# Kernel tuning notes

Measured on AMD Instinct MI355X. Metric: run time of the kernel, lower is better.

Reference implementation:

```python
import jax, jax.numpy as jnp
import numpy as np

DIM = 2048
H = 16           # n_heads
KV = 4           # n_kv_heads
G = H // KV      # gqa factor
CQ = 128         # q_compressed_dim
QN, QR = 96, 32  # q nope / rope head dims
CKV = 128        # kv_compressed_dim
KN, KR = 64, 64  # k nope / rope head dims
VD = 256         # v_head_dim
THETA = 10000.0


def _t5_layer_norm(x, gamma, eps=1e-5):
    mu = jnp.mean(x, axis=-1, keepdims=True)
    var = jnp.var(x, axis=-1, keepdims=True)
    return (x - mu) * jax.lax.rsqrt(var + eps) * gamma


def _rope(x):
    # x: [B, H, S, D] with interleaved even/odd rotation, positions = arange(S)
    S, D = x.shape[-2], x.shape[-1]
    inv_freq = 1.0 / THETA ** (jnp.arange(0, D, 2, dtype=jnp.float32) / D)
    ang = jnp.arange(S, dtype=jnp.float32)[:, None] * inv_freq  # [S, D/2]
    cos = jnp.cos(ang).astype(x.dtype)
    sin = jnp.sin(ang).astype(x.dtype)
    xe, xo = x[..., ::2], x[..., 1::2]
    re = xe * cos - xo * sin
    ro = xe * sin + xo * cos
    return jnp.stack((re, ro), axis=-1).reshape(x.shape)


def setup_inputs() -> dict:
    key = jax.random.key(0)
    ks = jax.random.split(key, 7)
    s = 0.02
    return {
        "x": jax.random.normal(ks[0], (2, 2048, DIM), dtype=jnp.float32),
        "w_dq": jax.random.normal(ks[1], (DIM, CQ), dtype=jnp.float32) * s,
        "gamma_q": jnp.ones((CQ,), dtype=jnp.float32),
        "w_uq": jax.random.normal(ks[2], (CQ, H * (QN + QR)), dtype=jnp.float32) * s,
        "w_dkv": jax.random.normal(ks[3], (DIM, CKV + KR), dtype=jnp.float32) * s,
        "gamma_kv": jnp.ones((CKV,), dtype=jnp.float32),
        "w_ukv": jax.random.normal(ks[4], (CKV, KV * (KN + VD)), dtype=jnp.float32) * s,
        "w_o": jax.random.normal(ks[5], (H * VD, DIM), dtype=jnp.float32) * s,
    }


def reference(x, w_dq, gamma_q, w_uq, w_dkv, gamma_kv, w_ukv, w_o):
    B, S, _ = x.shape
    # low-rank Q path
    cq = _t5_layer_norm(x @ w_dq, gamma_q)                     # [B,S,CQ]
    q = cq @ w_uq                                              # [B,S,H*(QN+QR)]
    q_nope = q[..., : H * QN].reshape(B, S, H, QN).transpose(0, 2, 1, 3)
    q_rope = q[..., H * QN :].reshape(B, S, H, QR).transpose(0, 2, 1, 3)
    q_rope = _rope(q_rope)
    q_states = jnp.concatenate((q_nope, q_rope), axis=-1)      # [B,H,S,QN+QR]

    # low-rank KV path + decoupled shared rope key
    ckv_kr = x @ w_dkv                                         # [B,S,CKV+KR]
    ckv = _t5_layer_norm(ckv_kr[..., :CKV], gamma_kv)
    k_rope = _rope(ckv_kr[..., CKV:][:, None, :, :])           # [B,1,S,KR]
    kv = ckv @ w_ukv                                           # [B,S,KV*(KN+VD)]
    k_nope = kv[..., : KV * KN].reshape(B, S, KV, KN).transpose(0, 2, 1, 3)
    v_states = kv[..., KV * KN :].reshape(B, S, KV, VD).transpose(0, 2, 1, 3)
    k_states = jnp.concatenate(
        (k_nope, jnp.broadcast_to(k_rope, (B, KV, S, KR))), axis=-1
    )                                                          # [B,KV,S,KN+KR]

    # grouped-query attention: broadcast kv heads instead of materializing repeats
    dqk = QN + QR  # == KN + KR == 128
    qg = q_states.reshape(B, KV, G, S, dqk)
    scores = jnp.einsum("bgrqd,bgkd->bgrqk", qg, k_states) / jnp.sqrt(
        jnp.asarray(dqk, dtype=x.dtype)
    )
    causal = jnp.triu(jnp.ones((S, S), dtype=bool), k=1)
    scores = jnp.where(causal, -jnp.inf, scores)
    attn = jax.nn.softmax(scores, axis=-1)
    out = jnp.einsum("bgrqk,bgkv->bgrqv", attn, v_states)      # [B,KV,G,S,VD]
    out = out.reshape(B, H, S, VD).transpose(0, 2, 1, 3).reshape(B, S, H * VD)
    return out @ w_o
```

## Files before the change

kernel.cpp:

```cpp
#include <hip/hip_runtime.h>
#include <hip/hip_bf16.h>
#include <math.h>

#define DIM   2048
#define S_LEN 2048
#define BATCH 2
#define NH    16
#define NKV   4
#define CQ_   128
#define QN_   96
#define QR_   32
#define CKV_  128
#define KN_   64
#define KR_   64
#define VD_   256
#define ROWS_TOT (BATCH*S_LEN)
#define QK_SCALE 0.08838834764831845f
#define LOG2E    1.4426950408889634f

typedef __attribute__((ext_vector_type(8)))  short short8;
typedef __attribute__((ext_vector_type(4)))  short short4v;
typedef __attribute__((ext_vector_type(4)))  float float4v;
typedef __attribute__((ext_vector_type(16))) float float16v;
typedef __attribute__((ext_vector_type(4)))  int   int4v;

__device__ inline short f2bf(float x) {
    union { __hip_bfloat16 h; short s; } u;
    u.h = __float2bfloat16(x);
    return u.s;
}

__device__ __forceinline__ void gl_lds16(const short* g, short* lds) {
    __builtin_amdgcn_global_load_lds(
        (const __attribute__((address_space(1))) unsigned int*)(g),
        (__attribute__((address_space(3))) unsigned int*)(lds),
        16, 0, 0);
}


__global__ __launch_bounds__(256)
void kprep_all(const float* __restrict__ w_o, const float* __restrict__ w_uq,
               const float* __restrict__ w_ukv, const float* __restrict__ w_dq,
               const float* __restrict__ w_dkv,
               short* __restrict__ w_oT, short* __restrict__ w_uqT,
               short* __restrict__ w_ukvT, short* __restrict__ wdT,
               float* __restrict__ tq, float* __restrict__ tk)
{
    const int bid = blockIdx.x, tid = threadIdx.x;
    if (bid >= 2312) {
        int gid = (bid - 2312) * 256 + tid;
        int spos = gid / 48, e = gid - spos * 48;
        if (e < 16) {
            float inv = powf(10000.f, -(float)(2 * e) / 32.f);
            float sn, c; sincosf((float)spos * inv, &sn, &c);
            tq[(spos * 16 + e) * 2 + 0] = c;
            tq[(spos * 16 + e) * 2 + 1] = sn;
        } else {
            int i2 = e - 16;
            float inv = powf(10000.f, -(float)(2 * i2) / 64.f);
            float sn, c; sincosf((float)spos * inv, &sn, &c);
            tk[(spos * 32 + i2) * 2 + 0] = c;
            tk[(spos * 32 + i2) * 2 + 1] = sn;
        }
        return;
    }

    __shared__ float tf[64][65];
    int lb, nct, R; short* dst;
    if (bid < 2048)      { lb = bid;        nct = 32; R = 4096; dst = w_oT;   }
    else if (bid < 2112) { lb = bid - 2048; nct = 32; R = 128;  dst = w_uqT;  }
    else if (bid < 2152) { lb = bid - 2112; nct = 20; R = 128;  dst = w_ukvT; }
    else                 { lb = bid - 2152; nct = 5;  R = 2048; dst = wdT;    }
    const int ct = lb % nct, rt = lb / nct;
    const int r0 = rt * 64, c0 = ct * 64;
    const float* src; int stride, nbase;
    if (bid < 2048)      { src = w_o;   stride = 2048; nbase = c0; }
    else if (bid < 2112) { src = w_uq;  stride = 2048; nbase = c0; }
    else if (bid < 2152) { src = w_ukv; stride = 1280; nbase = c0; }
    else if (ct < 2)     { src = w_dq;  stride = 128;  nbase = c0; }
    else                 { src = w_dkv; stride = 192;  nbase = c0 - 128; }

    #pragma unroll
    for (int u4 = 0; u4 < 4; ++u4) {
        int u = u4 * 256 + tid;
        int kr = u >> 4, nc = (u & 15) * 4;
        float4 v = *reinterpret_cast<const float4*>(&src[(size_t)(r0 + kr) * stride + nbase + nc]);
        tf[kr][nc + 0] = v.x; tf[kr][nc + 1] = v.y;
        tf[kr][nc + 2] = v.z; tf[kr][nc + 3] = v.w;
    }
    __syncthreads();
    #pragma unroll
    for (int u2 = 0; u2 < 2; ++u2) {
        int u = u2 * 256 + tid;
        int nr = u >> 3, kc8 = (u & 7) * 8;
        short8 o;
        #pragma unroll
        for (int j = 0; j < 8; ++j) o[j] = f2bf(tf[kc8 + j][nr]);
        *reinterpret_cast<short8*>(&dst[(size_t)(c0 + nr) * R + r0 + kc8]) = o;
    }
}

__global__ __launch_bounds__(256)
void k1_mfma(const float* __restrict__ x, const short* __restrict__ wdT,
             const float* __restrict__ gamma_q, const float* __restrict__ gamma_kv,
             const float* __restrict__ tk,
             short* __restrict__ cq_bf, short* __restrict__ ckv_bf,
             float* __restrict__ kr_rope)
{
    __shared__ float ys[16][321];
    __shared__ float st[16][4];
    const int tid = threadIdx.x, lane = tid & 63, w = tid >> 6;
    const int g = lane >> 4, l15 = lane & 15;
    const int m0 = blockIdx.x * 16;
    const int wn0 = w * 80;

    float4v acc[5];
    #pragma unroll
    for (int nj = 0; nj < 5; ++nj) acc[nj] = (float4v){0.f, 0.f, 0.f, 0.f};

    const float* arow = x + (size_t)(m0 + l15) * 2048 + g * 8;
    for (int ks = 0; ks < 64; ++ks) {
        float4 a0 = *reinterpret_cast<const float4*>(arow + ks * 32);
        float4 a1 = *reinterpret_cast<const float4*>(arow + ks * 32 + 4);
        short8 a;
        a[0] = f2bf(a0.x); a[1] = f2bf(a0.y); a[2] = f2bf(a0.z); a[3] = f2bf(a0.w);
        a[4] = f2bf(a1.x); a[5] = f2bf(a1.y); a[6] = f2bf(a1.z); a[7] = f2bf(a1.w);
        #pragma unroll
        for (int nj = 0; nj < 5; ++nj) {
            short8 bf = *reinterpret_cast<const short8*>(
                wdT + (size_t)(wn0 + nj * 16 + l15) * 2048 + ks * 32 + g * 8);
            acc[nj] = __builtin_amdgcn_mfma_f32_16x16x32_bf16(a, bf, acc[nj], 0, 0, 0);
        }
    }

    #pragma unroll
    for (int nj = 0; nj < 5; ++nj)
        #pragma unroll
        for (int r = 0; r < 4; ++r)
            ys[g * 4 + r][wn0 + nj * 16 + l15] = acc[nj][r];
    __syncthreads();

    if (tid < 32) {
        int row = tid >> 1, seg = tid & 1, base = seg * 128;
        float s1 = 0.f, s2 = 0.f;
        for (int j = 0; j < 128; ++j) { float v = ys[row][base + j]; s1 += v; s2 += v * v; }
        float mu  = s1 * (1.f / 128.f);
        float var = s2 * (1.f / 128.f) - mu * mu;
        st[row][seg * 2 + 0] = mu;
        st[row][seg * 2 + 1] = rsqrtf(var + 1e-5f);
    }
    __syncthreads();

    for (int i = tid; i < 16 * 320; i += 256) {
        int row = i / 320, col = i - row * 320;
        int r = m0 + row, spos = r & (S_LEN - 1);
        float v = ys[row][col];
        if (col < 128) {
            cq_bf[(size_t)r * CQ_ + col] =
                f2bf((v - st[row][0]) * st[row][1] * gamma_q[col] * (QK_SCALE * LOG2E));
        } else if (col < 256) {
            ckv_bf[(size_t)r * CKV_ + (col - 128)] =
                f2bf((v - st[row][2]) * st[row][3] * gamma_kv[col - 128]);
        } else {
            int d = col - 256, i2 = d >> 1;
            float xe = ys[row][256 + (d & ~1)];
            float xo = ys[row][256 + (d | 1)];
            float c  = tk[(spos * 32 + i2) * 2 + 0];
            float sn = tk[(spos * 32 + i2) * 2 + 1];
            kr_rope[(size_t)r * KR_ + d] = (d & 1) ? (xe * sn + xo * c)
                                                   : (xe * c - xo * sn);
        }
    }
}

__global__ __launch_bounds__(256)
void k2_mfma(const short* __restrict__ cq_bf, const short* __restrict__ w_uqT,
             const float* __restrict__ tq, short* __restrict__ q_states)
{
    const int tid = threadIdx.x, lane = tid & 63, w = tid >> 6;
    const int g = lane >> 4, l15 = lane & 15;
    const int bm = blockIdx.x >> 1, ns = blockIdx.x & 1;
    const int m0 = bm * 16;
    const int nb = ns * 1024 + w * 256;

    short8 af[4];
    #pragma unroll
    for (int ks = 0; ks < 4; ++ks)
        af[ks] = *reinterpret_cast<const short8*>(
            cq_bf + (size_t)(m0 + l15) * 128 + ks * 32 + g * 8);

    float4v acc[16];
    #pragma unroll
    for (int nj = 0; nj < 16; ++nj) acc[nj] = (float4v){0.f, 0.f, 0.f, 0.f};

    #pragma unroll
    for (int ks = 0; ks < 4; ++ks)
        #pragma unroll
        for (int nj = 0; nj < 16; ++nj) {
            short8 bf = *reinterpret_cast<const short8*>(
                w_uqT + (size_t)(nb + nj * 16 + l15) * 128 + ks * 32 + g * 8);
            acc[nj] = __builtin_amdgcn_mfma_f32_16x16x32_bf16(af[ks], bf, acc[nj], 0, 0, 0);
        }

    #pragma unroll
    for (int nj = 0; nj < 16; ++nj) {
        int j = nb + nj * 16 + l15;
        if (j < NH * QN_) {
            int h = j / QN_, d = j - h * QN_;
            #pragma unroll
            for (int r = 0; r < 4; ++r) {
                int rg = m0 + g * 4 + r, bb = rg >> 11, spos = rg & (S_LEN - 1);
                q_states[(((size_t)bb * NH + h) * S_LEN + spos) * 128 + d] =
                    f2bf(acc[nj][r]);
            }
        } else {
            int jj = j - NH * QN_;
            int h = jj >> 5, d = jj & 31, i2 = d >> 1;
            #pragma unroll
            for (int r = 0; r < 4; ++r) {
                int rg = m0 + g * 4 + r, bb = rg >> 11, spos = rg & (S_LEN - 1);
                float v = acc[nj][r];
                float p = __shfl_xor(v, 1, 64);
                float c  = tq[(spos * 16 + i2) * 2 + 0];
                float sn = tq[(spos * 16 + i2) * 2 + 1];
                float out = (d & 1) ? (p * sn + v * c) : (v * c - p * sn);
                q_states[(((size_t)bb * NH + h) * S_LEN + spos) * 128 + QN_ + d] =
                    f2bf(out);
            }
        }
    }
}

__global__ __launch_bounds__(256)
void k3_mfma(const short* __restrict__ ckv_bf, const short* __restrict__ w_ukvT,
             const float* __restrict__ kr_rope,
             short* __restrict__ k_frag, short* __restrict__ v_states)
{
    const int tid = threadIdx.x, lane = tid & 63, w = tid >> 6;
    const int g = lane >> 4, l15 = lane & 15;
    const int m0 = blockIdx.x * 16;
    const int nb = w * 320;

    short8 af[4];
    #pragma unroll
    for (int ks = 0; ks < 4; ++ks)
        af[ks] = *reinterpret_cast<const short8*>(
            ckv_bf + (size_t)(m0 + l15) * 128 + ks * 32 + g * 8);

    float4v acc[20];
    #pragma unroll
    for (int nj = 0; nj < 20; ++nj) acc[nj] = (float4v){0.f, 0.f, 0.f, 0.f};

    #pragma unroll
    for (int ks = 0; ks < 4; ++ks)
        #pragma unroll
        for (int nj = 0; nj < 20; ++nj) {
            short8 bf = *reinterpret_cast<const short8*>(
                w_ukvT + (size_t)(nb + nj * 16 + l15) * 128 + ks * 32 + g * 8);
            acc[nj] = __builtin_amdgcn_mfma_f32_16x16x32_bf16(af[ks], bf, acc[nj], 0, 0, 0);
        }

    #pragma unroll
    for (int nj = 0; nj < 20; ++nj) {
        int j = nb + nj * 16 + l15;
        if (j < NKV * KN_) {
            int kvh = j >> 6, d = j & 63;
            int stf = d >> 4, hif = (d >> 3) & 1, jo = d & 7;
            #pragma unroll
            for (int r = 0; r < 4; ++r) {
                int rg = m0 + g * 4 + r, bb = rg >> 11, spos = rg & (S_LEN - 1);
                int bk = bb * NKV + kvh;
                size_t idx = ((size_t)(bk * 32 + (spos >> 6)) * 1024
                              + ((spos >> 5) & 1) * 512 + stf * 64 + hif * 32
                              + (spos & 31)) * 8 + jo;
                k_frag[idx] = f2bf(acc[nj][r]);
            }
        } else {
            int jj = j - NKV * KN_;
            int kvh = jj >> 8, d = jj & 255;
            #pragma unroll
            for (int r = 0; r < 4; ++r) {
                int rg = m0 + g * 4 + r, bb = rg >> 11, spos = rg & (S_LEN - 1);
                v_states[(((size_t)bb * NKV + kvh) * S_LEN + spos) * VD_ + d] =
                    f2bf(acc[nj][r]);
            }
        }
    }

    for (int i = tid; i < 16 * KR_; i += 256) {
        int rr = i >> 6, dd = i & 63;
        int rg = m0 + rr, bb = rg >> 11, spos = rg & (S_LEN - 1);
        short vv = f2bf(kr_rope[(size_t)rg * KR_ + dd]);
        int d = 64 + dd;
        int stf = d >> 4, hif = (d >> 3) & 1, jo = d & 7;
        size_t ubase = ((size_t)(spos >> 6)) * 1024
                       + ((spos >> 5) & 1) * 512 + stf * 64 + hif * 32 + (spos & 31);
        #pragma unroll
        for (int kvh = 0; kvh < NKV; ++kvh) {
            int bk = bb * NKV + kvh;
            k_frag[((size_t)bk * 32 * 1024 + ubase) * 8 + jo] = vv;
        }
    }
}

__global__ __launch_bounds__(256)
void k3t_transpose_v(const short* __restrict__ v, short* __restrict__ v_frag)
{
    __shared__ short t[64][66];
    const int tid = threadIdx.x;
    const int vtile = blockIdx.x & 3;
    const int stile = (blockIdx.x >> 2) & 31;
    const int bk    = blockIdx.x >> 7;

    const short* src = v + ((size_t)bk * S_LEN + stile * 64) * VD_ + vtile * 64;
    #pragma unroll
    for (int u2 = 0; u2 < 2; ++u2) {
        int u = u2 * 256 + tid;
        int srow = u >> 3, vc8 = (u & 7) * 8;
        short8 val = *reinterpret_cast<const short8*>(src + (size_t)srow * VD_ + vc8);
        #pragma unroll
        for (int j = 0; j < 8; ++j) t[srow][vc8 + j] = val[j];
    }
    __syncthreads();
    short* dstbase = v_frag + (size_t)(bk * 32 + stile) * 16384;
    #pragma unroll
    for (int u2 = 0; u2 < 2; ++u2) {
        int u = u2 * 256 + tid;
        int vr = u >> 3, sc8 = (u & 7) * 8;
        short8 o;
        #pragma unroll
        for (int j = 0; j < 8; ++j) o[j] = t[sc8 + j][vr];
        int d = vtile * 64 + vr;
        int dt = d >> 5, l31d = d & 31;
        int half = sc8 >> 5, ksf = (sc8 >> 4) & 1, hif = (sc8 >> 3) & 1;
        size_t idx16 = (size_t)dt * 256 + half * 128 + ksf * 64 + hif * 32 + l31d;
        *reinterpret_cast<short8*>(dstbase + idx16 * 8) = o;
    }
}

__global__ __launch_bounds__(512, 1)
void k4_attn_mfma(const short* __restrict__ q_states,
                  const short* __restrict__ k_frag,
                  const short* __restrict__ v_frag,
                  short* __restrict__ attn_out)
{
    __shared__ __align__(16) short ks_lds[3][8192];
    __shared__ __align__(16) short vt_lds[2][16384];

    const int tid = threadIdx.x, lane = tid & 63, w = tid >> 6;
    const int l31 = lane & 31, hi = lane >> 5;
    const int g = w & 3, h = w >> 2;
    const int bid = blockIdx.x;
    const int qt = (bid < 256) ? (15 - (bid >> 5)) : (7 - ((bid - 256) >> 5));
    const int bh = bid & 31;
    const int h_head = bh & 15, b = bh >> 4, kvh = h_head >> 2;
    const int bk = b * NKV + kvh;

    const short* kfbase = k_frag + (size_t)bk * 32 * 8192;
    const short* vfbase = v_frag + (size_t)bk * 32 * 16384;

    const int qrow0 = qt * 128 + g * 32;
    const int qglob = qrow0 + l31;

    short8 qcur[8];
    {
        const short* qr = q_states +
            (((size_t)b * NH + h_head) * S_LEN + qrow0 + l31) * 128 + hi * 8;
        #pragma unroll
        for (int st = 0; st < 8; ++st)
            qcur[st] = *reinterpret_cast<const short8*>(qr + st * 16);
    }

    float16v o[8];
    #pragma unroll
    for (int dt = 0; dt < 8; ++dt)
        #pragma unroll
        for (int r = 0; r < 16; ++r) o[dt][r] = 0.f;
    float mreg = -1e30f, lreg = 0.f;

    const int nkt = 2 * (qt + 1);

    auto issueK = [&](int kt, int bufi) {
        const short* src = kfbase + (size_t)kt * 8192;
        #pragma unroll
        for (int i = 0; i < 2; ++i) {
            int c = w * 2 + i;
            gl_lds16(src + c * 512 + lane * 8, &ks_lds[bufi][c * 512]);
        }
    };
    auto issueV = [&](int kt, int bufi) {
        const short* src = vfbase + (size_t)kt * 16384;
        #pragma unroll
        for (int i = 0; i < 4; ++i) {
            int c = w * 4 + i;
            gl_lds16(src + c * 512 + lane * 8, &vt_lds[bufi][c * 512]);
        }
    };

    issueK(0, 0);
    issueV(0, 0);
    issueK(1, 1);

    for (int seq = 0; seq < nkt; ++seq) {
        if (seq < nkt - 1) { asm volatile("s_waitcnt vmcnt(2)" ::: "memory"); }
        else               { asm volatile("s_waitcnt vmcnt(0)" ::: "memory"); }
        __builtin_amdgcn_s_barrier();
        __builtin_amdgcn_sched_barrier(0);

        if (seq + 1 < nkt) issueV(seq + 1, (seq + 1) & 1);
        if (seq + 2 < nkt) issueK(seq + 2, (seq + 2) % 3);

        const int kvb = seq * 64 + h * 32;
        if (kvb <= qrow0 + 31) {
            const short* kbuf = &ks_lds[seq % 3][h * 4096];
            float16v s;
            #pragma unroll
            for (int r = 0; r < 16; ++r) s[r] = 0.f;
            __builtin_amdgcn_s_setprio(1);
            #pragma unroll
            for (int st = 0; st < 8; ++st) {
                short8 kf = *reinterpret_cast<const short8*>(kbuf + st * 512 + lane * 8);
                s = __builtin_amdgcn_mfma_f32_32x32x16_bf16(kf, qcur[st], s, 0, 0, 0);
            }
            __builtin_amdgcn_s_setprio(0);

            if (kvb + 31 > qglob - (l31 == 31 ? 0 : 0)) {
                #pragma unroll
                for (int r = 0; r < 16; ++r) {
                    int kc = kvb + ((r & 3) + 8 * (r >> 2) + 4 * hi);
                    if (kc > qglob) s[r] = -1e30f;
                }
            }

            float mx = s[0];
            #pragma unroll
            for (int r = 1; r < 16; ++r) mx = fmaxf(mx, s[r]);
            mx = fmaxf(mx, __shfl_xor(mx, 32, 64));
            bool need = mx > mreg + 8.f;
            if (__ballot(need)) {
                float mnew = fmaxf(mreg, mx);
                float corr = exp2f(mreg - mnew);
                mreg = mnew;
                lreg *= corr;
                #pragma unroll
                for (int dt = 0; dt < 8; ++dt)
                    #pragma unroll
                    for (int r = 0; r < 16; ++r) o[dt][r] *= corr;
            }
            #pragma unroll
            for (int r = 0; r < 16; ++r) s[r] = exp2f(s[r] - mreg);
            float ps = 0.f;
            #pragma unroll
            for (int r = 0; r < 16; ++r) ps += s[r];
            ps += __shfl_xor(ps, 32, 64);
            lreg += ps;

            const short* vbuf = &vt_lds[seq & 1][h * 1024];
            __builtin_amdgcn_s_setprio(1);
            #pragma unroll
            for (int ks = 0; ks < 2; ++ks) {
                const int rb = ks * 8;
                int c01, c23, c45, c67;
                asm("v_cvt_pk_bf16_f32 %0, %1, %2" : "=v"(c01) : "v"(s[rb+0]), "v"(s[rb+1]));
                asm("v_cvt_pk_bf16_f32 %0, %1, %2" : "=v"(c23) : "v"(s[rb+2]), "v"(s[rb+3]));
                asm("v_cvt_pk_bf16_f32 %0, %1, %2" : "=v"(c45) : "v"(s[rb+4]), "v"(s[rb+5]));
                asm("v_cvt_pk_bf16_f32 %0, %1, %2" : "=v"(c67) : "v"(s[rb+6]), "v"(s[rb+7]));
                asm("v_permlane32_swap_b32 %0, %1" : "+v"(c01), "+v"(c45));
                asm("v_permlane32_swap_b32 %0, %1" : "+v"(c23), "+v"(c67));
                union { int4v i4; short8 s8; } u_;
                u_.i4.x = c01; u_.i4.y = c23; u_.i4.z = c45; u_.i4.w = c67;
                short8 pa = u_.s8;
                #pragma unroll
                for (int dt = 0; dt < 8; ++dt) {
                    short8 vf = *reinterpret_cast<const short8*>(
                        vbuf + dt * 2048 + ks * 512 + lane * 8);
                    o[dt] = __builtin_amdgcn_mfma_f32_32x32x16_bf16(vf, pa, o[dt], 0, 0, 0);
                }
            }
            __builtin_amdgcn_s_setprio(0);
        }
    }

    __syncthreads();
    {
        float* mlb = (float*)(&ks_lds[0][0]);
        mlb[w * 64 + lane] = mreg;
        mlb[512 + w * 64 + lane] = lreg;
    }
    __syncthreads();
    float s0f = 0.f, s1f = 0.f;
    if (h == 0) {
        float* mlb = (float*)(&ks_lds[0][0]);
        float m1 = mlb[(w + 4) * 64 + lane];
        float l1 = mlb[512 + (w + 4) * 64 + lane];
        float ms = fmaxf(mreg, m1);
        float c0 = exp2f(mreg - ms), c1 = exp2f(m1 - ms);
        float ls = lreg * c0 + l1 * c1;
        s0f = c0 / ls; s1f = c1 / ls;
    }
    float* cb = (float*)(&ks_lds[0][0]) + 1024;
    short* obase = attn_out + (((size_t)b * S_LEN + qglob) * NH + h_head) * VD_;
    for (int dt = 0; dt < 8; ++dt) {
        __syncthreads();
        if (h == 1) {
            #pragma unroll
            for (int r = 0; r < 16; ++r)
                cb[r * 256 + g * 64 + lane] = o[dt][r];
        }
        __syncthreads();
        if (h == 0) {
            #pragma unroll
            for (int r = 0; r < 16; ++r)
                o[dt][r] = o[dt][r] * s0f + cb[r * 256 + g * 64 + lane] * s1f;
            #pragma unroll
            for (int k4i = 0; k4i < 4; ++k4i) {
                int d0 = dt * 32 + k4i * 8 + hi * 4;
                short4v pk;
                #pragma unroll
                for (int j = 0; j < 4; ++j) pk[j] = f2bf(o[dt][k4i * 4 + j]);
                *reinterpret_cast<short4v*>(obase + d0) = pk;
            }
        }
    }
}

__global__ __launch_bounds__(256)
void k5_gemm_mfma(const short* __restrict__ A,
                  const short* __restrict__ Bt,
                  float* __restrict__ C)
{
    __shared__ __align__(16) short at[128 * 64];
    __shared__ __align__(16) short bt[128 * 64];
    const int tid  = threadIdx.x;
    const int lane = tid & 63;
    const int wid  = tid >> 6;
    const int wm = wid >> 1, wn = wid & 1;
    const int g = lane >> 4, l15 = lane & 15;
    const int wg = (blockIdx.x & 7) * 64 + (blockIdx.x >> 3);
    const int bn = wg & 15, bm = wg >> 4;
    const int m0 = bm * 128, n0 = bn * 128;

    float4v acc[4][4];
    #pragma unroll
    for (int mi = 0; mi < 4; ++mi)
        #pragma unroll
        for (int nj = 0; nj < 4; ++nj) acc[mi][nj] = (float4v){0.f, 0.f, 0.f, 0.f};

    for (int k0 = 0; k0 < 4096; k0 += 64) {
        __syncthreads();
        #pragma unroll
        for (int i = 0; i < 4; ++i) {
            int row = wid * 32 + i * 8 + (lane >> 3);
            int ch  = lane & 7;
            gl_lds16(A + (size_t)(m0 + row) * 4096 + k0 + ((ch ^ (row & 7)) * 8),
                     at + wid * 2048 + i * 512);
            gl_lds16(Bt + (size_t)(n0 + row) * 4096 + k0 + ((ch ^ (row & 7)) * 8),
                     bt + wid * 2048 + i * 512);
        }
        __syncthreads();

        #pragma unroll
        for (int kb = 0; kb < 2; ++kb) {
            short8 af[4], bfr[4];
            #pragma unroll
            for (int mi = 0; mi < 4; ++mi) {
                int row = wm * 64 + mi * 16 + l15;
                af[mi] = *reinterpret_cast<const short8*>(
                    at + row * 64 + (((g + 4 * kb) ^ (row & 7)) * 8));
            }
            #pragma unroll
            for (int nj = 0; nj < 4; ++nj) {
                int row = wn * 64 + nj * 16 + l15;
                bfr[nj] = *reinterpret_cast<const short8*>(
                    bt + row * 64 + (((g + 4 * kb) ^ (row & 7)) * 8));
            }
            #pragma unroll
            for (int mi = 0; mi < 4; ++mi)
                #pragma unroll
                for (int nj = 0; nj < 4; ++nj)
                    acc[mi][nj] = __builtin_amdgcn_mfma_f32_16x16x32_bf16(
                        af[mi], bfr[nj], acc[mi][nj], 0, 0, 0);
        }
    }

    #pragma unroll
    for (int mi = 0; mi < 4; ++mi)
        #pragma unroll
        for (int nj = 0; nj < 4; ++nj)
            #pragma unroll
            for (int r = 0; r < 4; ++r)
                C[(size_t)(m0 + wm * 64 + mi * 16 + g * 4 + r) * DIM + n0 + wn * 64 + nj * 16 + l15] =
                    acc[mi][nj][r];
}

extern "C" void kernel_launch(void* const* d_in, const int* in_sizes, int n_in,
                              void* d_out, int out_size, void* d_ws, size_t ws_size,
                              hipStream_t stream)
{
    const float* x        = (const float*)d_in[0];
    const float* w_dq     = (const float*)d_in[1];
    const float* gamma_q  = (const float*)d_in[2];
    const float* w_uq     = (const float*)d_in[3];
    const float* w_dkv    = (const float*)d_in[4];
    const float* gamma_kv = (const float*)d_in[5];
    const float* w_ukv    = (const float*)d_in[6];
    const float* w_o      = (const float*)d_in[7];
    float* out = (float*)d_out;

    char* ws = (char*)d_ws;
    float* kr_rope  = (float*)(ws);
    short* cq_bf    = (short*)(ws + (1ull  << 20));
    short* ckv_bf   = (short*)(ws + (2ull  << 20));
    float* tq       = (float*)(ws + (3ull  << 20));
    float* tk       = (float*)(ws + (4ull  << 20));
    short* w_uqT    = (short*)(ws + (5ull  << 20));
    short* w_ukvT   = (short*)(ws + (6ull  << 20));
    short* wdT      = (short*)(ws + (7ull  << 20));
    short* q_states = (short*)(ws + (9ull  << 20));
    short* k_frag   = (short*)(ws + (25ull << 20));
    short* v_states = (short*)(ws + (29ull << 20));
    short* v_frag   = (short*)(ws + (37ull << 20));
    short* attn_out = (short*)(ws + (45ull << 20));
    short* w_oT     = (short*)(ws + (77ull << 20));

    kprep_all<<<dim3(2696), dim3(256), 0, stream>>>(
        w_o, w_uq, w_ukv, w_dq, w_dkv, w_oT, w_uqT, w_ukvT, wdT, tq, tk);

    k1_mfma<<<dim3(ROWS_TOT / 16), dim3(256), 0, stream>>>(
        x, wdT, gamma_q, gamma_kv, tk, cq_bf, ckv_bf, kr_rope);

    k2_mfma<<<dim3((ROWS_TOT / 16) * 2), dim3(256), 0, stream>>>(
        cq_bf, w_uqT, tq, q_states);

    k3_mfma<<<dim3(ROWS_TOT / 16), dim3(256), 0, stream>>>(
        ckv_bf, w_ukvT, kr_rope, k_frag, v_states);

    k3t_transpose_v<<<dim3(BATCH * NKV * 32 * 4), dim3(256), 0, stream>>>(
        v_states, v_frag);

    k4_attn_mfma<<<dim3(512), dim3(512), 0, stream>>>(
        q_states, k_frag, v_frag, attn_out);

    k5_gemm_mfma<<<dim3((ROWS_TOT / 128) * (DIM / 128)), dim3(256), 0, stream>>>(
        attn_out, w_oT, out);
}
```

Baseline: 262.5 us.

## Fuse Q/KV up-projections, write V fragments directly, pre-convert x, split QK MFMA chains

Several changes land together. x is converted to bf16 in the prep kernel so k1 loads half the bytes. The Q and KV up-projection kernels are merged into one launch, and the KV path writes V straight into the attention fragment layout, which drops the separate transpose kernel and the v_states round trip. The attention QK^T loop now uses two independent accumulator chains to reduce MFMA dependency stalls, and the causal mask is applied only near the diagonal. The output GEMM tile ordering is also reswizzled. The trade-offs are an extra bf16 x buffer with its write and reread, and scattered 2-byte stores for V.

```diff
diff --git a/kernel.cpp b/kernel.cpp
--- a/kernel.cpp
+++ b/kernel.cpp
@@ -39,16 +39,27 @@
 
 
 __global__ __launch_bounds__(256)
-void kprep_all(const float* __restrict__ w_o, const float* __restrict__ w_uq,
-               const float* __restrict__ w_ukv, const float* __restrict__ w_dq,
-               const float* __restrict__ w_dkv,
-               short* __restrict__ w_oT, short* __restrict__ w_uqT,
-               short* __restrict__ w_ukvT, short* __restrict__ wdT,
-               float* __restrict__ tq, float* __restrict__ tk)
+void kprep_all(const float* __restrict__ x, const float* __restrict__ w_o,
+               const float* __restrict__ w_uq, const float* __restrict__ w_ukv,
+               const float* __restrict__ w_dq, const float* __restrict__ w_dkv,
+               short* __restrict__ xbf, short* __restrict__ w_oT,
+               short* __restrict__ w_uqT, short* __restrict__ w_ukvT,
+               short* __restrict__ wdT, float* __restrict__ tq,
+               float* __restrict__ tk)
 {
     const int bid = blockIdx.x, tid = threadIdx.x;
-    if (bid >= 2312) {
-        int gid = (bid - 2312) * 256 + tid;
+    if (bid < 4096) {
+        int i = bid * 2048 + tid * 8;
+        float4 a = *reinterpret_cast<const float4*>(x + i);
+        float4 b = *reinterpret_cast<const float4*>(x + i + 4);
+        short8 o;
+        o[0] = f2bf(a.x); o[1] = f2bf(a.y); o[2] = f2bf(a.z); o[3] = f2bf(a.w);
+        o[4] = f2bf(b.x); o[5] = f2bf(b.y); o[6] = f2bf(b.z); o[7] = f2bf(b.w);
+        *reinterpret_cast<short8*>(xbf + i) = o;
+        return;
+    }
+    if (bid >= 6408) {
+        int gid = (bid - 6408) * 256 + tid;
         int spos = gid / 48, e = gid - spos * 48;
         if (e < 16) {
             float inv = powf(10000.f, -(float)(2 * e) / 32.f);
@@ -66,19 +77,20 @@
     }
 
     __shared__ float tf[64][65];
+    const int tb = bid - 4096;
     int lb, nct, R; short* dst;
-    if (bid < 2048)      { lb = bid;        nct = 32; R = 4096; dst = w_oT;   }
-    else if (bid < 2112) { lb = bid - 2048; nct = 32; R = 128;  dst = w_uqT;  }
-    else if (bid < 2152) { lb = bid - 2112; nct = 20; R = 128;  dst = w_ukvT; }
-    else                 { lb = bid - 2152; nct = 5;  R = 2048; dst = wdT;    }
+    if (tb < 2048)      { lb = tb;        nct = 32; R = 4096; dst = w_oT;   }
+    else if (tb < 2112) { lb = tb - 2048; nct = 32; R = 128;  dst = w_uqT;  }
+    else if (tb < 2152) { lb = tb - 2112; nct = 20; R = 128;  dst = w_ukvT; }
+    else                { lb = tb - 2152; nct = 5;  R = 2048; dst = wdT;    }
     const int ct = lb % nct, rt = lb / nct;
     const int r0 = rt * 64, c0 = ct * 64;
     const float* src; int stride, nbase;
-    if (bid < 2048)      { src = w_o;   stride = 2048; nbase = c0; }
-    else if (bid < 2112) { src = w_uq;  stride = 2048; nbase = c0; }
-    else if (bid < 2152) { src = w_ukv; stride = 1280; nbase = c0; }
-    else if (ct < 2)     { src = w_dq;  stride = 128;  nbase = c0; }
-    else                 { src = w_dkv; stride = 192;  nbase = c0 - 128; }
+    if (tb < 2048)      { src = w_o;   stride = 2048; nbase = c0; }
+    else if (tb < 2112) { src = w_uq;  stride = 2048; nbase = c0; }
+    else if (tb < 2152) { src = w_ukv; stride = 1280; nbase = c0; }
+    else if (ct < 2)    { src = w_dq;  stride = 128;  nbase = c0; }
+    else                { src = w_dkv; stride = 192;  nbase = c0 - 128; }
 
     #pragma unroll
     for (int u4 = 0; u4 < 4; ++u4) {
@@ -101,7 +113,7 @@
 }
 
 __global__ __launch_bounds__(256)
-void k1_mfma(const float* __restrict__ x, const short* __restrict__ wdT,
+void k1_mfma(const short* __restrict__ xbf, const short* __restrict__ wdT,
              const float* __restrict__ gamma_q, const float* __restrict__ gamma_kv,
              const float* __restrict__ tk,
              short* __restrict__ cq_bf, short* __restrict__ ckv_bf,
@@ -118,13 +130,9 @@
     #pragma unroll
     for (int nj = 0; nj < 5; ++nj) acc[nj] = (float4v){0.f, 0.f, 0.f, 0.f};
 
-    const float* arow = x + (size_t)(m0 + l15) * 2048 + g * 8;
+    const short* arow = xbf + (size_t)(m0 + l15) * 2048 + g * 8;
     for (int ks = 0; ks < 64; ++ks) {
-        float4 a0 = *reinterpret_cast<const float4*>(arow + ks * 32);
-        float4 a1 = *reinterpret_cast<const float4*>(arow + ks * 32 + 4);
-        short8 a;
-        a[0] = f2bf(a0.x); a[1] = f2bf(a0.y); a[2] = f2bf(a0.z); a[3] = f2bf(a0.w);
-        a[4] = f2bf(a1.x); a[5] = f2bf(a1.y); a[6] = f2bf(a1.z); a[7] = f2bf(a1.w);
+        short8 a = *reinterpret_cast<const short8*>(arow + ks * 32);
         #pragma unroll
         for (int nj = 0; nj < 5; ++nj) {
             short8 bf = *reinterpret_cast<const short8*>(
@@ -174,167 +182,134 @@
 }
 
 __global__ __launch_bounds__(256)
-void k2_mfma(const short* __restrict__ cq_bf, const short* __restrict__ w_uqT,
-             const float* __restrict__ tq, short* __restrict__ q_states)
+void k23_fused(const short* __restrict__ cq_bf, const short* __restrict__ w_uqT,
+               const float* __restrict__ tq, short* __restrict__ q_states,
+               const short* __restrict__ ckv_bf, const short* __restrict__ w_ukvT,
+               const float* __restrict__ kr_rope,
+               short* __restrict__ k_frag, short* __restrict__ v_frag)
 {
     const int tid = threadIdx.x, lane = tid & 63, w = tid >> 6;
     const int g = lane >> 4, l15 = lane & 15;
-    const int bm = blockIdx.x >> 1, ns = blockIdx.x & 1;
-    const int m0 = bm * 16;
-    const int nb = ns * 1024 + w * 256;
-
-    short8 af[4];
-    #pragma unroll
-    for (int ks = 0; ks < 4; ++ks)
-        af[ks] = *reinterpret_cast<const short8*>(
-            cq_bf + (size_t)(m0 + l15) * 128 + ks * 32 + g * 8);
-
-    float4v acc[16];
-    #pragma unroll
-    for (int nj = 0; nj < 16; ++nj) acc[nj] = (float4v){0.f, 0.f, 0.f, 0.f};
-
-    #pragma unroll
-    for (int ks = 0; ks < 4; ++ks)
+
+    if (blockIdx.x < 512) {
+        const int bm = blockIdx.x >> 1, ns = blockIdx.x & 1;
+        const int m0 = bm * 16;
+        const int nb = ns * 1024 + w * 256;
+
+        short8 af[4];
+        #pragma unroll
+        for (int ks = 0; ks < 4; ++ks)
+            af[ks] = *reinterpret_cast<const short8*>(
+                cq_bf + (size_t)(m0 + l15) * 128 + ks * 32 + g * 8);
+
+        float4v acc[16];
+        #pragma unroll
+        for (int nj = 0; nj < 16; ++nj) acc[nj] = (float4v){0.f, 0.f, 0.f, 0.f};
+
+        #pragma unroll
+        for (int ks = 0; ks < 4; ++ks)
+            #pragma unroll
+            for (int nj = 0; nj < 16; ++nj) {
+                short8 bf = *reinterpret_cast<const short8*>(
+                    w_uqT + (size_t)(nb + nj * 16 + l15) * 128 + ks * 32 + g * 8);
+                acc[nj] = __builtin_amdgcn_mfma_f32_16x16x32_bf16(af[ks], bf, acc[nj], 0, 0, 0);
+            }
+
         #pragma unroll
         for (int nj = 0; nj < 16; ++nj) {
-            short8 bf = *reinterpret_cast<const short8*>(
-                w_uqT + (size_t)(nb + nj * 16 + l15) * 128 + ks * 32 + g * 8);
-            acc[nj] = __builtin_amdgcn_mfma_f32_16x16x32_bf16(af[ks], bf, acc[nj], 0, 0, 0);
-        }
-
-    #pragma unroll
-    for (int nj = 0; nj < 16; ++nj) {
-        int j = nb + nj * 16 + l15;
-        if (j < NH * QN_) {
-            int h = j / QN_, d = j - h * QN_;
-            #pragma unroll
-            for (int r = 0; r < 4; ++r) {
-                int rg = m0 + g * 4 + r, bb = rg >> 11, spos = rg & (S_LEN - 1);
-                q_states[(((size_t)bb * NH + h) * S_LEN + spos) * 128 + d] =
-                    f2bf(acc[nj][r]);
-            }
-        } else {
-            int jj = j - NH * QN_;
-            int h = jj >> 5, d = jj & 31, i2 = d >> 1;
-            #pragma unroll
-            for (int r = 0; r < 4; ++r) {
-                int rg = m0 + g * 4 + r, bb = rg >> 11, spos = rg & (S_LEN - 1);
-                float v = acc[nj][r];
-                float p = __shfl_xor(v, 1, 64);
-                float c  = tq[(spos * 16 + i2) * 2 + 0];
-                float sn = tq[(spos * 16 + i2) * 2 + 1];
-                float out = (d & 1) ? (p * sn + v * c) : (v * c - p * sn);
-                q_states[(((size_t)bb * NH + h) * S_LEN + spos) * 128 + QN_ + d] =
-                    f2bf(out);
-            }
-        }
-    }
-}
-
-__global__ __launch_bounds__(256)
-void k3_mfma(const short* __restrict__ ckv_bf, const short* __restrict__ w_ukvT,
-             const float* __restrict__ kr_rope,
-             short* __restrict__ k_frag, short* __restrict__ v_states)
-{
-    const int tid = threadIdx.x, lane = tid & 63, w = tid >> 6;
-    const int g = lane >> 4, l15 = lane & 15;
-    const int m0 = blockIdx.x * 16;
-    const int nb = w * 320;
-
-    short8 af[4];
-    #pragma unroll
-    for (int ks = 0; ks < 4; ++ks)
-        af[ks] = *reinterpret_cast<const short8*>(
-            ckv_bf + (size_t)(m0 + l15) * 128 + ks * 32 + g * 8);
-
-    float4v acc[20];
-    #pragma unroll
-    for (int nj = 0; nj < 20; ++nj) acc[nj] = (float4v){0.f, 0.f, 0.f, 0.f};
-
-    #pragma unroll
-    for (int ks = 0; ks < 4; ++ks)
+            int j = nb + nj * 16 + l15;
+            if (j < NH * QN_) {
+                int h = j / QN_, d = j - h * QN_;
+                #pragma unroll
+                for (int r = 0; r < 4; ++r) {
+                    int rg = m0 + g * 4 + r, bb = rg >> 11, spos = rg & (S_LEN - 1);
+                    q_states[(((size_t)bb * NH + h) * S_LEN + spos) * 128 + d] =
+                        f2bf(acc[nj][r]);
+                }
+            } else {
+                int jj = j - NH * QN_;
+                int h = jj >> 5, d = jj & 31, i2 = d >> 1;
+                #pragma unroll
+                for (int r = 0; r < 4; ++r) {
+                    int rg = m0 + g * 4 + r, bb = rg >> 11, spos = rg & (S_LEN - 1);
+                    float v = acc[nj][r];
+                    float p = __shfl_xor(v, 1, 64);
+                    float c  = tq[(spos * 16 + i2) * 2 + 0];
+                    float sn = tq[(spos * 16 + i2) * 2 + 1];
+                    float out = (d & 1) ? (p * sn + v * c) : (v * c - p * sn);
+                    q_states[(((size_t)bb * NH + h) * S_LEN + spos) * 128 + QN_ + d] =
+                        f2bf(out);
+                }
+            }
+        }
+    } else {
+        const int m0 = (blockIdx.x - 512) * 16;
+        const int nb = w * 320;
+
+        short8 af[4];
+        #pragma unroll
+        for (int ks = 0; ks < 4; ++ks)
+            af[ks] = *reinterpret_cast<const short8*>(
+                ckv_bf + (size_t)(m0 + l15) * 128 + ks * 32 + g * 8);
+
+        float4v acc[20];
+        #pragma unroll
+        for (int nj = 0; nj < 20; ++nj) acc[nj] = (float4v){0.f, 0.f, 0.f, 0.f};
+
+        #pragma unroll
+        for (int ks = 0; ks < 4; ++ks)
+            #pragma unroll
+            for (int nj = 0; nj < 20; ++nj) {
+                short8 bf = *reinterpret_cast<const short8*>(
+                    w_ukvT + (size_t)(nb + nj * 16 + l15) * 128 + ks * 32 + g * 8);
+                acc[nj] = __builtin_amdgcn_mfma_f32_16x16x32_bf16(af[ks], bf, acc[nj], 0, 0, 0);
+            }
+
         #pragma unroll
         for (int nj = 0; nj < 20; ++nj) {
-            short8 bf = *reinterpret_cast<const short8*>(
-                w_ukvT + (size_t)(nb + nj * 16 + l15) * 128 + ks * 32 + g * 8);
-            acc[nj] = __builtin_amdgcn_mfma_f32_16x16x32_bf16(af[ks], bf, acc[nj], 0, 0, 0);
-        }
-
-    #pragma unroll
-    for (int nj = 0; nj < 20; ++nj) {
-        int j = nb + nj * 16 + l15;
-        if (j < NKV * KN_) {
-            int kvh = j >> 6, d = j & 63;
+            int j = nb + nj * 16 + l15;
+            if (j < NKV * KN_) {
+                int kvh = j >> 6, d = j & 63;
+                int stf = d >> 4, hif = (d >> 3) & 1, jo = d & 7;
+                #pragma unroll
+                for (int r = 0; r < 4; ++r) {
+                    int rg = m0 + g * 4 + r, bb = rg >> 11, spos = rg & (S_LEN - 1);
+                    int bk = bb * NKV + kvh;
+                    size_t idx = ((size_t)(bk * 32 + (spos >> 6)) * 1024
+                                  + ((spos >> 5) & 1) * 512 + stf * 64 + hif * 32
+                                  + (spos & 31)) * 8 + jo;
+                    k_frag[idx] = f2bf(acc[nj][r]);
+                }
+            } else {
+                int jj = j - NKV * KN_;
+                int kvh = jj >> 8, d = jj & 255;
+                int dt5 = d >> 5, l31d = d & 31;
+                #pragma unroll
+                for (int r = 0; r < 4; ++r) {
+                    int rg = m0 + g * 4 + r, bb = rg >> 11, spos = rg & (S_LEN - 1);
+                    int bk = bb * NKV + kvh;
+                    size_t slot = (size_t)(bk * 32 + (spos >> 6)) * 2048
+                                  + dt5 * 256 + ((spos & 63) >> 5) * 128
+                                  + ((spos >> 4) & 1) * 64 + ((spos >> 3) & 1) * 32 + l31d;
+                    v_frag[slot * 8 + (spos & 7)] = f2bf(acc[nj][r]);
+                }
+            }
+        }
+
+        for (int i = tid; i < 16 * KR_; i += 256) {
+            int rr = i >> 6, dd = i & 63;
+            int rg = m0 + rr, bb = rg >> 11, spos = rg & (S_LEN - 1);
+            short vv = f2bf(kr_rope[(size_t)rg * KR_ + dd]);
+            int d = 64 + dd;
             int stf = d >> 4, hif = (d >> 3) & 1, jo = d & 7;
-            #pragma unroll
-            for (int r = 0; r < 4; ++r) {
-                int rg = m0 + g * 4 + r, bb = rg >> 11, spos = rg & (S_LEN - 1);
+            size_t ubase = ((size_t)(spos >> 6)) * 1024
+                           + ((spos >> 5) & 1) * 512 + stf * 64 + hif * 32 + (spos & 31);
+            #pragma unroll
+            for (int kvh = 0; kvh < NKV; ++kvh) {
                 int bk = bb * NKV + kvh;
-                size_t idx = ((size_t)(bk * 32 + (spos >> 6)) * 1024
-                              + ((spos >> 5) & 1) * 512 + stf * 64 + hif * 32
-                              + (spos & 31)) * 8 + jo;
-                k_frag[idx] = f2bf(acc[nj][r]);
-            }
-        } else {
-            int jj = j - NKV * KN_;
-            int kvh = jj >> 8, d = jj & 255;
-            #pragma unroll
-            for (int r = 0; r < 4; ++r) {
-                int rg = m0 + g * 4 + r, bb = rg >> 11, spos = rg & (S_LEN - 1);
-                v_states[(((size_t)bb * NKV + kvh) * S_LEN + spos) * VD_ + d] =
-                    f2bf(acc[nj][r]);
-            }
-        }
-    }
-
-    for (int i = tid; i < 16 * KR_; i += 256) {
-        int rr = i >> 6, dd = i & 63;
-        int rg = m0 + rr, bb = rg >> 11, spos = rg & (S_LEN - 1);
-        short vv = f2bf(kr_rope[(size_t)rg * KR_ + dd]);
-        int d = 64 + dd;
-        int stf = d >> 4, hif = (d >> 3) & 1, jo = d & 7;
-        size_t ubase = ((size_t)(spos >> 6)) * 1024
-                       + ((spos >> 5) & 1) * 512 + stf * 64 + hif * 32 + (spos & 31);
-        #pragma unroll
-        for (int kvh = 0; kvh < NKV; ++kvh) {
-            int bk = bb * NKV + kvh;
-            k_frag[((size_t)bk * 32 * 1024 + ubase) * 8 + jo] = vv;
-        }
-    }
-}
-
-__global__ __launch_bounds__(256)
-void k3t_transpose_v(const short* __restrict__ v, short* __restrict__ v_frag)
-{
-    __shared__ short t[64][66];
-    const int tid = threadIdx.x;
-    const int vtile = blockIdx.x & 3;
-    const int stile = (blockIdx.x >> 2) & 31;
-    const int bk    = blockIdx.x >> 7;
-
-    const short* src = v + ((size_t)bk * S_LEN + stile * 64) * VD_ + vtile * 64;
-    #pragma unroll
-    for (int u2 = 0; u2 < 2; ++u2) {
-        int u = u2 * 256 + tid;
-        int srow = u >> 3, vc8 = (u & 7) * 8;
-        short8 val = *reinterpret_cast<const short8*>(src + (size_t)srow * VD_ + vc8);
-        #pragma unroll
-        for (int j = 0; j < 8; ++j) t[srow][vc8 + j] = val[j];
-    }
-    __syncthreads();
-    short* dstbase = v_frag + (size_t)(bk * 32 + stile) * 16384;
-    #pragma unroll
-    for (int u2 = 0; u2 < 2; ++u2) {
-        int u = u2 * 256 + tid;
-        int vr = u >> 3, sc8 = (u & 7) * 8;
-        short8 o;
-        #pragma unroll
-        for (int j = 0; j < 8; ++j) o[j] = t[sc8 + j][vr];
-        int d = vtile * 64 + vr;
-        int dt = d >> 5, l31d = d & 31;
-        int half = sc8 >> 5, ksf = (sc8 >> 4) & 1, hif = (sc8 >> 3) & 1;
-        size_t idx16 = (size_t)dt * 256 + half * 128 + ksf * 64 + hif * 32 + l31d;
-        *reinterpret_cast<short8*>(dstbase + idx16 * 8) = o;
+                k_frag[((size_t)bk * 32 * 1024 + ubase) * 8 + jo] = vv;
+            }
+        }
     }
 }
 
@@ -413,22 +388,29 @@
         const int kvb = seq * 64 + h * 32;
         if (kvb <= qrow0 + 31) {
             const short* kbuf = &ks_lds[seq % 3][h * 4096];
+            float16v sa, sb;
+            #pragma unroll
+            for (int r = 0; r < 16; ++r) { sa[r] = 0.f; sb[r] = 0.f; }
+            __builtin_amdgcn_s_setprio(1);
+            #pragma unroll
+            for (int st = 0; st < 8; st += 2) {
+                short8 kf0 = *reinterpret_cast<const short8*>(kbuf + st * 512 + lane * 8);
+                sa = __builtin_amdgcn_mfma_f32_32x32x16_bf16(kf0, qcur[st], sa, 0, 0, 0);
+                short8 kf1 = *reinterpret_cast<const short8*>(kbuf + (st + 1) * 512 + lane * 8);
+                sb = __builtin_amdgcn_mfma_f32_32x32x16_bf16(kf1, qcur[st + 1], sb, 0, 0, 0);
+            }
+            __builtin_amdgcn_s_setprio(0);
             float16v s;
             #pragma unroll
-            for (int r = 0; r < 16; ++r) s[r] = 0.f;
-            __builtin_amdgcn_s_setprio(1);
-            #pragma unroll
-            for (int st = 0; st < 8; ++st) {
-                short8 kf = *reinterpret_cast<const short8*>(kbuf + st * 512 + lane * 8);
-                s = __builtin_amdgcn_mfma_f32_32x32x16_bf16(kf, qcur[st], s, 0, 0, 0);
-            }
-            __builtin_amdgcn_s_setprio(0);
-
-            if (kvb + 31 > qglob - (l31 == 31 ? 0 : 0)) {
-                #pragma unroll
-                for (int r = 0; r < 16; ++r) {
-                    int kc = kvb + ((r & 3) + 8 * (r >> 2) + 4 * hi);
-                    if (kc > qglob) s[r] = -1e30f;
+            for (int r = 0; r < 16; ++r) s[r] = sa[r] + sb[r];
+
+            if (kvb + 31 > qglob || kvb + 31 > qrow0 + 31) {
+                if (kvb + 31 > qrow0) {
+                    #pragma unroll
+                    for (int r = 0; r < 16; ++r) {
+                        int kc = kvb + ((r & 3) + 8 * (r >> 2) + 4 * hi);
+                        if (kc > qglob) s[r] = -1e30f;
+                    }
                 }
             }
 
@@ -536,8 +518,8 @@
     const int wid  = tid >> 6;
     const int wm = wid >> 1, wn = wid & 1;
     const int g = lane >> 4, l15 = lane & 15;
-    const int wg = (blockIdx.x & 7) * 64 + (blockIdx.x >> 3);
-    const int bn = wg & 15, bm = wg >> 4;
+    const int swz = (blockIdx.x & 7) * 64 + (blockIdx.x >> 3);
+    const int bm = swz & 31, bn = swz >> 5;
     const int m0 = bm * 128, n0 = bn * 128;
 
     float4v acc[4][4];
@@ -618,29 +600,24 @@
     short* wdT      = (short*)(ws + (7ull  << 20));
     short* q_states = (short*)(ws + (9ull  << 20));
     short* k_frag   = (short*)(ws + (25ull << 20));
-    short* v_states = (short*)(ws + (29ull << 20));
-    short* v_frag   = (short*)(ws + (37ull << 20));
-    short* attn_out = (short*)(ws + (45ull << 20));
-    short* w_oT     = (short*)(ws + (77ull << 20));
-
-    kprep_all<<<dim3(2696), dim3(256), 0, stream>>>(
-        w_o, w_uq, w_ukv, w_dq, w_dkv, w_oT, w_uqT, w_ukvT, wdT, tq, tk);
+    short* v_frag   = (short*)(ws + (29ull << 20));
+    short* attn_out = (short*)(ws + (37ull << 20));
+    short* w_oT     = (short*)(ws + (69ull << 20));
+    short* xbf      = (short*)(ws + (85ull << 20));
+
+    kprep_all<<<dim3(6792), dim3(256), 0, stream>>>(
+        x, w_o, w_uq, w_ukv, w_dq, w_dkv,
+        xbf, w_oT, w_uqT, w_ukvT, wdT, tq, tk);
 
     k1_mfma<<<dim3(ROWS_TOT / 16), dim3(256), 0, stream>>>(
-        x, wdT, gamma_q, gamma_kv, tk, cq_bf, ckv_bf, kr_rope);
-
-    k2_mfma<<<dim3((ROWS_TOT / 16) * 2), dim3(256), 0, stream>>>(
-        cq_bf, w_uqT, tq, q_states);
-
-    k3_mfma<<<dim3(ROWS_TOT / 16), dim3(256), 0, stream>>>(
-        ckv_bf, w_ukvT, kr_rope, k_frag, v_states);
-
-    k3t_transpose_v<<<dim3(BATCH * NKV * 32 * 4), dim3(256), 0, stream>>>(
-        v_states, v_frag);
+        xbf, wdT, gamma_q, gamma_kv, tk, cq_bf, ckv_bf, kr_rope);
+
+    k23_fused<<<dim3(768), dim3(256), 0, stream>>>(
+        cq_bf, w_uqT, tq, q_states, ckv_bf, w_ukvT, kr_rope, k_frag, v_frag);
 
     k4_attn_mfma<<<dim3(512), dim3(512), 0, stream>>>(
         q_states, k_frag, v_frag, attn_out);
 
-    k5_gemm_mfma<<<dim3((ROWS_TOT / 128) * (DIM / 128)), dim3(256), 0, stream>>>(
+    k5_gemm_mfma<<<dim3(512), dim3(256), 0, stream>>>(
         attn_out, w_oT, out);
 }
```

Measured after the change: 269.0 us. 2.5% more time.

## Overlap w_o transpose with attention, pre-convert x to bf16, split QK accumulators

Applied to the files above, without the earlier changes.

The w_o fp32→bf16 transpose moves out of the prep kernel and into 1024 extra blocks appended to the attention launch, so it can fill CUs left idle by the causal attention tail. The prep kernel now converts x to bf16 once, and k1 reads bf16 directly instead of converting inside its K loop. The QK MFMA chain in attention is split into two independent accumulators to shorten the dependency chain. The causal-mask condition is simplified, and the output GEMM's block swizzle is changed to iterate M-major. The cost is an extra bf16 copy of x written to and read from global memory, and larger attention grids whose extra blocks compete for LDS and occupancy.

```diff
diff --git a/kernel.cpp b/kernel.cpp
--- a/kernel.cpp
+++ b/kernel.cpp
@@ -39,16 +39,27 @@
 
 
 __global__ __launch_bounds__(256)
-void kprep_all(const float* __restrict__ w_o, const float* __restrict__ w_uq,
-               const float* __restrict__ w_ukv, const float* __restrict__ w_dq,
-               const float* __restrict__ w_dkv,
-               short* __restrict__ w_oT, short* __restrict__ w_uqT,
-               short* __restrict__ w_ukvT, short* __restrict__ wdT,
-               float* __restrict__ tq, float* __restrict__ tk)
+void kprep_all(const float* __restrict__ x,
+               const float* __restrict__ w_uq, const float* __restrict__ w_ukv,
+               const float* __restrict__ w_dq, const float* __restrict__ w_dkv,
+               short* __restrict__ xbf,
+               short* __restrict__ w_uqT, short* __restrict__ w_ukvT,
+               short* __restrict__ wdT, float* __restrict__ tq,
+               float* __restrict__ tk)
 {
     const int bid = blockIdx.x, tid = threadIdx.x;
-    if (bid >= 2312) {
-        int gid = (bid - 2312) * 256 + tid;
+    if (bid < 4096) {
+        int i = bid * 2048 + tid * 8;
+        float4 a = *reinterpret_cast<const float4*>(x + i);
+        float4 b = *reinterpret_cast<const float4*>(x + i + 4);
+        short8 o;
+        o[0] = f2bf(a.x); o[1] = f2bf(a.y); o[2] = f2bf(a.z); o[3] = f2bf(a.w);
+        o[4] = f2bf(b.x); o[5] = f2bf(b.y); o[6] = f2bf(b.z); o[7] = f2bf(b.w);
+        *reinterpret_cast<short8*>(xbf + i) = o;
+        return;
+    }
+    if (bid >= 4360) {
+        int gid = (bid - 4360) * 256 + tid;
         int spos = gid / 48, e = gid - spos * 48;
         if (e < 16) {
             float inv = powf(10000.f, -(float)(2 * e) / 32.f);
@@ -66,19 +77,18 @@
     }
 
     __shared__ float tf[64][65];
+    const int tb = bid - 4096;
     int lb, nct, R; short* dst;
-    if (bid < 2048)      { lb = bid;        nct = 32; R = 4096; dst = w_oT;   }
-    else if (bid < 2112) { lb = bid - 2048; nct = 32; R = 128;  dst = w_uqT;  }
-    else if (bid < 2152) { lb = bid - 2112; nct = 20; R = 128;  dst = w_ukvT; }
-    else                 { lb = bid - 2152; nct = 5;  R = 2048; dst = wdT;    }
+    if (tb < 64)       { lb = tb;       nct = 32; R = 128;  dst = w_uqT;  }
+    else if (tb < 104) { lb = tb - 64;  nct = 20; R = 128;  dst = w_ukvT; }
+    else               { lb = tb - 104; nct = 5;  R = 2048; dst = wdT;    }
     const int ct = lb % nct, rt = lb / nct;
     const int r0 = rt * 64, c0 = ct * 64;
     const float* src; int stride, nbase;
-    if (bid < 2048)      { src = w_o;   stride = 2048; nbase = c0; }
-    else if (bid < 2112) { src = w_uq;  stride = 2048; nbase = c0; }
-    else if (bid < 2152) { src = w_ukv; stride = 1280; nbase = c0; }
-    else if (ct < 2)     { src = w_dq;  stride = 128;  nbase = c0; }
-    else                 { src = w_dkv; stride = 192;  nbase = c0 - 128; }
+    if (tb < 64)       { src = w_uq;  stride = 2048; nbase = c0; }
+    else if (tb < 104) { src = w_ukv; stride = 1280; nbase = c0; }
+    else if (ct < 2)   { src = w_dq;  stride = 128;  nbase = c0; }
+    else               { src = w_dkv; stride = 192;  nbase = c0 - 128; }
 
     #pragma unroll
     for (int u4 = 0; u4 < 4; ++u4) {
@@ -101,7 +111,7 @@
 }
 
 __global__ __launch_bounds__(256)
-void k1_mfma(const float* __restrict__ x, const short* __restrict__ wdT,
+void k1_mfma(const short* __restrict__ xbf, const short* __restrict__ wdT,
              const float* __restrict__ gamma_q, const float* __restrict__ gamma_kv,
              const float* __restrict__ tk,
              short* __restrict__ cq_bf, short* __restrict__ ckv_bf,
@@ -118,13 +128,9 @@
     #pragma unroll
     for (int nj = 0; nj < 5; ++nj) acc[nj] = (float4v){0.f, 0.f, 0.f, 0.f};
 
-    const float* arow = x + (size_t)(m0 + l15) * 2048 + g * 8;
+    const short* arow = xbf + (size_t)(m0 + l15) * 2048 + g * 8;
     for (int ks = 0; ks < 64; ++ks) {
-        float4 a0 = *reinterpret_cast<const float4*>(arow + ks * 32);
-        float4 a1 = *reinterpret_cast<const float4*>(arow + ks * 32 + 4);
-        short8 a;
-        a[0] = f2bf(a0.x); a[1] = f2bf(a0.y); a[2] = f2bf(a0.z); a[3] = f2bf(a0.w);
-        a[4] = f2bf(a1.x); a[5] = f2bf(a1.y); a[6] = f2bf(a1.z); a[7] = f2bf(a1.w);
+        short8 a = *reinterpret_cast<const short8*>(arow + ks * 32);
         #pragma unroll
         for (int nj = 0; nj < 5; ++nj) {
             short8 bf = *reinterpret_cast<const short8*>(
@@ -342,15 +348,45 @@
 void k4_attn_mfma(const short* __restrict__ q_states,
                   const short* __restrict__ k_frag,
                   const short* __restrict__ v_frag,
-                  short* __restrict__ attn_out)
+                  short* __restrict__ attn_out,
+                  const float* __restrict__ w_o,
+                  short* __restrict__ w_oT)
 {
     __shared__ __align__(16) short ks_lds[3][8192];
     __shared__ __align__(16) short vt_lds[2][16384];
 
     const int tid = threadIdx.x, lane = tid & 63, w = tid >> 6;
+    const int bid = blockIdx.x;
+
+    if (bid >= 512) {
+        const int sub = tid >> 8, t256 = tid & 255;
+        const int tile = (bid - 512) * 2 + sub;
+        const int ct = tile & 31, rt = tile >> 5;
+        const int r0 = rt * 64, c0 = ct * 64;
+        float* tfb = (float*)((char*)ks_lds + sub * 16832);
+        #pragma unroll
+        for (int u4 = 0; u4 < 4; ++u4) {
+            int u = u4 * 256 + t256;
+            int kr = u >> 4, nc = (u & 15) * 4;
+            float4 v = *reinterpret_cast<const float4*>(&w_o[(size_t)(r0 + kr) * DIM + c0 + nc]);
+            tfb[kr * 65 + nc + 0] = v.x; tfb[kr * 65 + nc + 1] = v.y;
+            tfb[kr * 65 + nc + 2] = v.z; tfb[kr * 65 + nc + 3] = v.w;
+        }
+        __syncthreads();
+        #pragma unroll
+        for (int u2 = 0; u2 < 2; ++u2) {
+            int u = u2 * 256 + t256;
+            int nr = u >> 3, kc8 = (u & 7) * 8;
+            short8 o;
+            #pragma unroll
+            for (int j = 0; j < 8; ++j) o[j] = f2bf(tfb[(kc8 + j) * 65 + nr]);
+            *reinterpret_cast<short8*>(&w_oT[(size_t)(c0 + nr) * 4096 + r0 + kc8]) = o;
+        }
+        return;
+    }
+
     const int l31 = lane & 31, hi = lane >> 5;
     const int g = w & 3, h = w >> 2;
-    const int bid = blockIdx.x;
     const int qt = (bid < 256) ? (15 - (bid >> 5)) : (7 - ((bid - 256) >> 5));
     const int bh = bid & 31;
     const int h_head = bh & 15, b = bh >> 4, kvh = h_head >> 2;
@@ -413,18 +449,23 @@
         const int kvb = seq * 64 + h * 32;
         if (kvb <= qrow0 + 31) {
             const short* kbuf = &ks_lds[seq % 3][h * 4096];
+            float16v sa, sb;
+            #pragma unroll
+            for (int r = 0; r < 16; ++r) { sa[r] = 0.f; sb[r] = 0.f; }
+            __builtin_amdgcn_s_setprio(1);
+            #pragma unroll
+            for (int st = 0; st < 8; st += 2) {
+                short8 kf0 = *reinterpret_cast<const short8*>(kbuf + st * 512 + lane * 8);
+                sa = __builtin_amdgcn_mfma_f32_32x32x16_bf16(kf0, qcur[st], sa, 0, 0, 0);
+                short8 kf1 = *reinterpret_cast<const short8*>(kbuf + (st + 1) * 512 + lane * 8);
+                sb = __builtin_amdgcn_mfma_f32_32x32x16_bf16(kf1, qcur[st + 1], sb, 0, 0, 0);
+            }
+            __builtin_amdgcn_s_setprio(0);
             float16v s;
             #pragma unroll
-            for (int r = 0; r < 16; ++r) s[r] = 0.f;
-            __builtin_amdgcn_s_setprio(1);
-            #pragma unroll
-            for (int st = 0; st < 8; ++st) {
-                short8 kf = *reinterpret_cast<const short8*>(kbuf + st * 512 + lane * 8);
-                s = __builtin_amdgcn_mfma_f32_32x32x16_bf16(kf, qcur[st], s, 0, 0, 0);
-            }
-            __builtin_amdgcn_s_setprio(0);
-
-            if (kvb + 31 > qglob - (l31 == 31 ? 0 : 0)) {
+            for (int r = 0; r < 16; ++r) s[r] = sa[r] + sb[r];
+
+            if (kvb + 31 > qrow0) {
                 #pragma unroll
                 for (int r = 0; r < 16; ++r) {
                     int kc = kvb + ((r & 3) + 8 * (r >> 2) + 4 * hi);
@@ -536,8 +577,8 @@
     const int wid  = tid >> 6;
     const int wm = wid >> 1, wn = wid & 1;
     const int g = lane >> 4, l15 = lane & 15;
-    const int wg = (blockIdx.x & 7) * 64 + (blockIdx.x >> 3);
-    const int bn = wg & 15, bm = wg >> 4;
+    const int swz = (blockIdx.x & 7) * 64 + (blockIdx.x >> 3);
+    const int bm = swz & 31, bn = swz >> 5;
     const int m0 = bm * 128, n0 = bn * 128;
 
     float4v acc[4][4];
@@ -622,12 +663,13 @@
     short* v_frag   = (short*)(ws + (37ull << 20));
     short* attn_out = (short*)(ws + (45ull << 20));
     short* w_oT     = (short*)(ws + (77ull << 20));
-
-    kprep_all<<<dim3(2696), dim3(256), 0, stream>>>(
-        w_o, w_uq, w_ukv, w_dq, w_dkv, w_oT, w_uqT, w_ukvT, wdT, tq, tk);
+    short* xbf      = (short*)(ws + (93ull << 20));
+
+    kprep_all<<<dim3(4744), dim3(256), 0, stream>>>(
+        x, w_uq, w_ukv, w_dq, w_dkv, xbf, w_uqT, w_ukvT, wdT, tq, tk);
 
     k1_mfma<<<dim3(ROWS_TOT / 16), dim3(256), 0, stream>>>(
-        x, wdT, gamma_q, gamma_kv, tk, cq_bf, ckv_bf, kr_rope);
+        xbf, wdT, gamma_q, gamma_kv, tk, cq_bf, ckv_bf, kr_rope);
 
     k2_mfma<<<dim3((ROWS_TOT / 16) * 2), dim3(256), 0, stream>>>(
         cq_bf, w_uqT, tq, q_states);
@@ -638,9 +680,9 @@
     k3t_transpose_v<<<dim3(BATCH * NKV * 32 * 4), dim3(256), 0, stream>>>(
         v_states, v_frag);
 
-    k4_attn_mfma<<<dim3(512), dim3(512), 0, stream>>>(
-        q_states, k_frag, v_frag, attn_out);
-
-    k5_gemm_mfma<<<dim3((ROWS_TOT / 128) * (DIM / 128)), dim3(256), 0, stream>>>(
+    k4_attn_mfma<<<dim3(1536), dim3(512), 0, stream>>>(
+        q_states, k_frag, v_frag, attn_out, w_o, w_oT);
+
+    k5_gemm_mfma<<<dim3(512), dim3(256), 0, stream>>>(
         attn_out, w_oT, out);
 }
```

Measured after the change: 276.2 us. +5.3%, slower.
